# Performance work log

Measured on AMD Instinct MI355X. Metric: run time of the kernel, lower is better.

The kernel has to match this reference:

```python
import jax, jax.numpy as jnp
import numpy as np

B, ENC_LEN, DEC_LEN = 4, 1024, 256
ENC_H, DEC_H, ATTN = 1024, 1024, 256


def setup_inputs() -> dict:
    key = jax.random.key(0)
    k1, k2, k3, k4, k5, k6 = jax.random.split(key, 6)
    scale = 0.02
    return {
        "encoded_seq": jax.random.normal(k1, (B, ENC_LEN, ENC_H), jnp.float32),
        "decoder_state": jax.random.normal(k2, (B, DEC_LEN, DEC_H), jnp.float32),
        "input_pad_mask": jnp.ones((B, ENC_LEN), jnp.float32),
        "Wh": jax.random.normal(k3, (ENC_H, ATTN), jnp.float32) * scale,
        "Ws": jax.random.normal(k4, (DEC_H, ATTN), jnp.float32) * scale,
        "bs": jax.random.normal(k5, (ATTN,), jnp.float32) * scale,
        "v": jax.random.normal(k6, (ATTN,), jnp.float32) * scale,
    }


def reference(encoded_seq, decoder_state, input_pad_mask, Wh, Ws, bs, v):
    # projections: [B, dec, A] and [B, enc, A]
    proj_dec = jnp.einsum('bdh,ha->bda', decoder_state, Ws) + bs
    proj_enc = jnp.einsum('beh,ha->bea', encoded_seq, Wh)
    # additive score: tanh(broadcast add) then dot with selector vector v
    added = jnp.tanh(proj_dec[:, :, None, :] + proj_enc[:, None, :, :])  # [B,dec,enc,A]
    attn_logits = jnp.einsum('bdea,a->bde', added, v)                    # [B,dec,enc]
    attn_weights = jax.nn.softmax(attn_logits, axis=-1)
    attn_weights2 = attn_weights * input_pad_mask[:, None, :]
    attn_renorm = attn_weights2 / jnp.sum(attn_weights2, axis=-1, keepdims=True)
    context = jnp.einsum('bde,beh->bdh', attn_renorm, encoded_seq)       # [B,dec,enc_h]
    return context, attn_renorm
```

## Files before the change

### kernel.cpp

```cpp
#include <hip/hip_runtime.h>
#include <hip/hip_bf16.h>

#define BB 4
#define ENC_LEN 1024
#define DEC_LEN 256
#define ENC_H 1024
#define ATTN_A 256

#define C2F 2.8853900817779268f

typedef short bf16x8 __attribute__((ext_vector_type(8)));
typedef float f32x4 __attribute__((ext_vector_type(4)));
typedef unsigned int u32x2 __attribute__((ext_vector_type(2)));

union Q2D {
  uint4 q;
  u32x2 d[2];
};
union BF8 {
  u32x2 d[2];
  bf16x8 v;
};

static __device__ __forceinline__ unsigned short f2bf(float x) {
  union {
    float f;
    unsigned int u;
  } c;
  c.f = x;
  unsigned int r = c.u + 0x7FFFu + ((c.u >> 16) & 1u);
  return (unsigned short)(r >> 16);
}

__global__ __launch_bounds__(256) void prep_k(
    const float* __restrict__ Wh, const float* __restrict__ Ws,
    const float* __restrict__ enc, const float* __restrict__ dec,
    unsigned short* __restrict__ WhT, unsigned short* __restrict__ WsT,
    unsigned short* __restrict__ encT, unsigned short* __restrict__ encB,
    unsigned short* __restrict__ decB) {
  __shared__ unsigned short T[64][68];
  const int wb = blockIdx.x;
  const int t = threadIdx.x;
  const int lr = t >> 4;
  const int lc4 = (t & 15) * 4;

  if (wb >= 1152) {
    const int q = wb - 1152;
    const int r0 = (q >> 4) * 64;
    const int c0 = (q & 15) * 64;
#pragma unroll
    for (int p = 0; p < 4; ++p) {
      const int r = lr + p * 16;
      const float4 v = *(const float4*)&dec[(long)(r0 + r) * ENC_H + c0 + lc4];
      ushort4 o;
      o.x = f2bf(v.x);
      o.y = f2bf(v.y);
      o.z = f2bf(v.z);
      o.w = f2bf(v.w);
      *(ushort4*)&decB[(long)(r0 + r) * ENC_H + c0 + lc4] = o;
    }
    return;
  }

  const float* in;
  unsigned short* out;
  unsigned short* out2 = nullptr;
  int R, C, bx, by;
  if (wb < 128) {
    in = (wb < 64) ? Wh : Ws;
    out = (wb < 64) ? WhT : WsT;
    const int tt = wb & 63;
    R = ENC_H;
    C = ATTN_A;
    bx = tt & 3;
    by = tt >> 2;
  } else {
    const int tt0 = wb - 128;
    const int b = tt0 >> 8;
    const int tt = tt0 & 255;
    in = enc + (long)b * ENC_LEN * ENC_H;
    out = encT + (long)b * ENC_H * ENC_LEN;
    out2 = encB + (long)b * ENC_LEN * ENC_H;
    R = ENC_LEN;
    C = ENC_H;
    bx = tt & 15;
    by = tt >> 4;
  }
  const int r0 = by * 64;
  const int c0 = bx * 64;

#pragma unroll
  for (int p = 0; p < 4; ++p) {
    const int r = lr + p * 16;
    const float4 v = *(const float4*)&in[(long)(r0 + r) * C + c0 + lc4];
    ushort4 o;
    o.x = f2bf(v.x);
    o.y = f2bf(v.y);
    o.z = f2bf(v.z);
    o.w = f2bf(v.w);
    *(ushort4*)&T[r][lc4] = o;
    if (out2) *(ushort4*)&out2[(long)(r0 + r) * C + c0 + lc4] = o;
  }
  __syncthreads();
#pragma unroll
  for (int p = 0; p < 4; ++p) {
    const int c = lr + p * 16;
    ushort4 o;
    o.x = T[lc4 + 0][c];
    o.y = T[lc4 + 1][c];
    o.z = T[lc4 + 2][c];
    o.w = T[lc4 + 3][c];
    *(ushort4*)&out[(long)(c0 + c) * R + r0 + lc4] = o;
  }
}

__global__ __launch_bounds__(256) void pgemm(const unsigned short* __restrict__ decB,
                                             const unsigned short* __restrict__ encB,
                                             const unsigned short* __restrict__ WsT,
                                             const unsigned short* __restrict__ WhT,
                                             float* __restrict__ pdP,
                                             float* __restrict__ peP) {
  __shared__ unsigned short As[64][36];
  __shared__ unsigned short Bs[64][36];
  __shared__ float Cs[64][68];

  const int s = blockIdx.z;
  const bool isPD = blockIdx.y < 16;
  const unsigned short* A = isPD ? decB : encB;
  const unsigned short* BT = isPD ? WsT : WhT;
  const int m0 = (isPD ? blockIdx.y : (blockIdx.y - 16)) * 64;
  const int n0 = blockIdx.x * 64;
  const int kb = s * 512;

  const int tid = threadIdx.x;
  const int lane = tid & 63;
  const int wave = tid >> 6;
  const int quad = lane >> 4;
  const int l16 = lane & 15;
  const int wm = (wave >> 1) * 32;
  const int wn = (wave & 1) * 32;
  const int sr = tid >> 2;
  const int sk = (tid & 3) * 8;

  f32x4 acc[2][2] = {{{0.f, 0.f, 0.f, 0.f}, {0.f, 0.f, 0.f, 0.f}},
                     {{0.f, 0.f, 0.f, 0.f}, {0.f, 0.f, 0.f, 0.f}}};

  const unsigned short* Ap = A + (long)(m0 + sr) * ENC_H + kb + sk;
  const unsigned short* Bp = BT + (long)(n0 + sr) * ENC_H + kb + sk;

  Q2D av, bv;
  av.q = *(const uint4*)(Ap);
  bv.q = *(const uint4*)(Bp);

  for (int k0 = 0; k0 < 512; k0 += 32) {
    __syncthreads();
    *(u32x2*)&As[sr][sk] = av.d[0];
    *(u32x2*)&As[sr][sk + 4] = av.d[1];
    *(u32x2*)&Bs[sr][sk] = bv.d[0];
    *(u32x2*)&Bs[sr][sk + 4] = bv.d[1];
    const int kn = (k0 + 32 < 512) ? (k0 + 32) : 0;
    av.q = *(const uint4*)(Ap + kn);
    bv.q = *(const uint4*)(Bp + kn);
    __syncthreads();

    bf16x8 af[2], bfr[2];
#pragma unroll
    for (int i = 0; i < 2; ++i) {
      BF8 t;
      t.d[0] = *(const u32x2*)&As[wm + i * 16 + l16][quad * 8];
      t.d[1] = *(const u32x2*)&As[wm + i * 16 + l16][quad * 8 + 4];
      af[i] = t.v;
    }
#pragma unroll
    for (int j = 0; j < 2; ++j) {
      BF8 t;
      t.d[0] = *(const u32x2*)&Bs[wn + j * 16 + l16][quad * 8];
      t.d[1] = *(const u32x2*)&Bs[wn + j * 16 + l16][quad * 8 + 4];
      bfr[j] = t.v;
    }
#pragma unroll
    for (int i = 0; i < 2; ++i)
#pragma unroll
      for (int j = 0; j < 2; ++j)
        acc[i][j] = __builtin_amdgcn_mfma_f32_16x16x32_bf16(af[i], bfr[j], acc[i][j],
                                                            0, 0, 0);
  }

  if (isPD) {
    float* out = pdP + (long)s * (1024 * ATTN_A);
#pragma unroll
    for (int j = 0; j < 2; ++j) {
      const int col = n0 + wn + j * 16 + l16;
#pragma unroll
      for (int i = 0; i < 2; ++i) {
        const int row = m0 + wm + i * 16 + quad * 4;
#pragma unroll
        for (int r = 0; r < 4; ++r)
          out[(long)(row + r) * ATTN_A + col] = C2F * acc[i][j][r];
      }
    }
  } else {
    __syncthreads();
#pragma unroll
    for (int i = 0; i < 2; ++i)
#pragma unroll
      for (int j = 0; j < 2; ++j)
#pragma unroll
        for (int r = 0; r < 4; ++r)
          Cs[wn + j * 16 + l16][wm + i * 16 + quad * 4 + r] = C2F * acc[i][j][r];
    __syncthreads();
    const int gb = m0 >> 10;
    const int e0 = m0 & 1023;
    float* out = peP + (long)s * (BB * ATTN_A * ENC_LEN);
#pragma unroll
    for (int p = 0; p < 4; ++p) {
      const int arow = (tid >> 4) + p * 16;
      const int e4 = (tid & 15) * 4;
      const float4 o = *(const float4*)&Cs[arow][e4];
      *(float4*)&out[(long)gb * (ATTN_A * ENC_LEN) + (long)(n0 + arow) * ENC_LEN +
                     e0 + e4] = o;
    }
  }
}

__global__ __launch_bounds__(256) void logits_k(const float* __restrict__ peP,
                                                const float* __restrict__ pdP,
                                                const float* __restrict__ v,
                                                const float* __restrict__ bs,
                                                float* __restrict__ p0,
                                                float* __restrict__ p1) {
  const int tid = threadIdx.x;
  const int e = blockIdx.x * 256 + tid;
  const int d0 = blockIdx.y * 8;
  const int b = blockIdx.z >> 1;
  const int a0 = (blockIdx.z & 1) * 128;

  __shared__ float Ed[128][8];
  __shared__ float vv[128];

  if (tid < 128) {
    const float cb = C2F * bs[a0 + tid];
#pragma unroll
    for (int dd = 0; dd < 8; ++dd) {
      const long idx = (long)(b * DEC_LEN + d0 + dd) * ATTN_A + a0 + tid;
      const float t = pdP[idx] + pdP[idx + 1024 * ATTN_A] + cb;
      Ed[tid][dd] = __builtin_amdgcn_exp2f(t);
    }
    vv[tid] = -2.0f * v[a0 + tid];
  }
  __syncthreads();

  float acc[8] = {0.f, 0.f, 0.f, 0.f, 0.f, 0.f, 0.f, 0.f};
  const float* pe0 = peP + (long)b * (ATTN_A * ENC_LEN) + (long)a0 * ENC_LEN + e;
  const float* pe1 = pe0 + (long)BB * ATTN_A * ENC_LEN;

  float pn0[4], pn1[4];
#pragma unroll
  for (int u = 0; u < 4; ++u) {
    pn0[u] = pe0[(long)u * ENC_LEN];
    pn1[u] = pe1[(long)u * ENC_LEN];
  }

  for (int a4 = 0; a4 < 128; a4 += 4) {
    float Ee[4];
#pragma unroll
    for (int u = 0; u < 4; ++u) Ee[u] = __builtin_amdgcn_exp2f(pn0[u] + pn1[u]);
    const int an = (a4 + 4 < 128) ? (a4 + 4) : 0;
#pragma unroll
    for (int u = 0; u < 4; ++u) {
      pn0[u] = pe0[(long)(an + u) * ENC_LEN];
      pn1[u] = pe1[(long)(an + u) * ENC_LEN];
    }
    const float4 v4 = *(const float4*)&vv[a4];

    float ed[4][8];
#pragma unroll
    for (int u = 0; u < 4; ++u) {
      const float4 e0v = *(const float4*)&Ed[a4 + u][0];
      const float4 e1v = *(const float4*)&Ed[a4 + u][4];
      ed[u][0] = e0v.x;
      ed[u][1] = e0v.y;
      ed[u][2] = e0v.z;
      ed[u][3] = e0v.w;
      ed[u][4] = e1v.x;
      ed[u][5] = e1v.y;
      ed[u][6] = e1v.z;
      ed[u][7] = e1v.w;
    }

#pragma unroll
    for (int dd = 0; dd < 8; ++dd) {
      const float dn0 = fmaf(ed[0][dd], Ee[0], 1.0f);
      const float dn1 = fmaf(ed[1][dd], Ee[1], 1.0f);
      const float dn2 = fmaf(ed[2][dd], Ee[2], 1.0f);
      const float dn3 = fmaf(ed[3][dd], Ee[3], 1.0f);
      const float x12 = dn0 * dn1;
      const float x34 = dn2 * dn3;
      float t1 = v4.x * dn1;
      t1 = fmaf(v4.y, dn0, t1);
      float t2 = v4.z * dn3;
      t2 = fmaf(v4.w, dn2, t2);
      float num = t1 * x34;
      num = fmaf(t2, x12, num);
      const float D = x12 * x34;
      const float r = __builtin_amdgcn_rcpf(D);
      acc[dd] = fmaf(num, r, acc[dd]);
    }
  }

  float* po = (blockIdx.z & 1) ? p1 : p0;
  const long base = ((long)(b * DEC_LEN + d0) * ENC_LEN) + e;
#pragma unroll
  for (int dd = 0; dd < 8; ++dd) po[base + (long)dd * ENC_LEN] = acc[dd];
}

__global__ __launch_bounds__(256) void softmax2_k(float* __restrict__ p0,
                                                  const float* __restrict__ p1,
                                                  const float* __restrict__ mask,
                                                  unsigned short* __restrict__ attnB) {
  const int row = blockIdx.x;
  const int b = row >> 8;
  const int tid = threadIdx.x;
  float* rp = p0 + (long)row * ENC_LEN;
  const float* rq = p1 + (long)row * ENC_LEN;
  const float* mp = mask + b * ENC_LEN;
  unsigned short* rb = attnB + (long)row * ENC_LEN;

  float l[4], m[4];
#pragma unroll
  for (int j = 0; j < 4; ++j) {
    l[j] = rp[tid + 256 * j] + rq[tid + 256 * j];
    m[j] = mp[tid + 256 * j];
  }

  __shared__ float redmax[4];
  __shared__ float redsum[4];
  const int lane = tid & 63;
  const int wid = tid >> 6;

  float tm = fmaxf(fmaxf(l[0], l[1]), fmaxf(l[2], l[3]));
#pragma unroll
  for (int off = 1; off < 64; off <<= 1) tm = fmaxf(tm, __shfl_xor(tm, off, 64));
  if (lane == 0) redmax[wid] = tm;
  __syncthreads();
  const float rmax = fmaxf(fmaxf(redmax[0], redmax[1]), fmaxf(redmax[2], redmax[3]));

  const float LOG2E = 1.4426950408889634f;
  float p[4];
  float ts = 0.f;
#pragma unroll
  for (int j = 0; j < 4; ++j) {
    p[j] = __builtin_amdgcn_exp2f((l[j] - rmax) * LOG2E) * m[j];
    ts += p[j];
  }
#pragma unroll
  for (int off = 1; off < 64; off <<= 1) ts += __shfl_xor(ts, off, 64);
  if (lane == 0) redsum[wid] = ts;
  __syncthreads();
  const float rsum = redsum[0] + redsum[1] + redsum[2] + redsum[3];

  const float inv = 1.0f / rsum;
#pragma unroll
  for (int j = 0; j < 4; ++j) {
    const float w = p[j] * inv;
    rp[tid + 256 * j] = w;
    rb[tid + 256 * j] = f2bf(w);
  }
}

__global__ __launch_bounds__(256) void cgemm(const unsigned short* __restrict__ attnB,
                                             const unsigned short* __restrict__ encT,
                                             float* __restrict__ cP) {
  __shared__ unsigned short As[64][36];
  __shared__ unsigned short Bs[64][36];

  const int b = blockIdx.z >> 1;
  const int s = blockIdx.z & 1;
  const int kb = s * 512;
  const unsigned short* A = attnB + (long)b * DEC_LEN * ENC_LEN;
  const unsigned short* BT = encT + (long)b * ENC_H * ENC_LEN;
  float* C = cP + (long)s * (BB * DEC_LEN * ENC_H) + (long)b * DEC_LEN * ENC_H;

  const int tid = threadIdx.x;
  const int lane = tid & 63;
  const int wave = tid >> 6;
  const int quad = lane >> 4;
  const int l16 = lane & 15;
  const int wm = (wave >> 1) * 32;
  const int wn = (wave & 1) * 32;
  const int m0 = blockIdx.y * 64;
  const int n0 = blockIdx.x * 64;
  const int sr = tid >> 2;
  const int sk = (tid & 3) * 8;

  f32x4 acc[2][2] = {{{0.f, 0.f, 0.f, 0.f}, {0.f, 0.f, 0.f, 0.f}},
                     {{0.f, 0.f, 0.f, 0.f}, {0.f, 0.f, 0.f, 0.f}}};

  const unsigned short* Ap = A + (long)(m0 + sr) * ENC_LEN + kb + sk;
  const unsigned short* Bp = BT + (long)(n0 + sr) * ENC_LEN + kb + sk;

  Q2D av, bv;
  av.q = *(const uint4*)(Ap);
  bv.q = *(const uint4*)(Bp);

  for (int k0 = 0; k0 < 512; k0 += 32) {
    __syncthreads();
    *(u32x2*)&As[sr][sk] = av.d[0];
    *(u32x2*)&As[sr][sk + 4] = av.d[1];
    *(u32x2*)&Bs[sr][sk] = bv.d[0];
    *(u32x2*)&Bs[sr][sk + 4] = bv.d[1];
    const int kn = (k0 + 32 < 512) ? (k0 + 32) : 0;
    av.q = *(const uint4*)(Ap + kn);
    bv.q = *(const uint4*)(Bp + kn);
    __syncthreads();

    bf16x8 af[2], bfr[2];
#pragma unroll
    for (int i = 0; i < 2; ++i) {
      BF8 t;
      t.d[0] = *(const u32x2*)&As[wm + i * 16 + l16][quad * 8];
      t.d[1] = *(const u32x2*)&As[wm + i * 16 + l16][quad * 8 + 4];
      af[i] = t.v;
    }
#pragma unroll
    for (int j = 0; j < 2; ++j) {
      BF8 t;
      t.d[0] = *(const u32x2*)&Bs[wn + j * 16 + l16][quad * 8];
      t.d[1] = *(const u32x2*)&Bs[wn + j * 16 + l16][quad * 8 + 4];
      bfr[j] = t.v;
    }
#pragma unroll
    for (int i = 0; i < 2; ++i)
#pragma unroll
      for (int j = 0; j < 2; ++j)
        acc[i][j] = __builtin_amdgcn_mfma_f32_16x16x32_bf16(af[i], bfr[j], acc[i][j],
                                                            0, 0, 0);
  }

#pragma unroll
  for (int j = 0; j < 2; ++j) {
    const int col = n0 + wn + j * 16 + l16;
#pragma unroll
    for (int i = 0; i < 2; ++i) {
      const int row = m0 + wm + i * 16 + quad * 4;
#pragma unroll
      for (int r = 0; r < 4; ++r) C[(long)(row + r) * ENC_H + col] = acc[i][j][r];
    }
  }
}

__global__ __launch_bounds__(256) void creduce(const float* __restrict__ cP,
                                               float* __restrict__ ctx) {
  const long i = ((long)blockIdx.x * 256 + threadIdx.x) * 4;
  const float4 x = *(const float4*)&cP[i];
  const float4 y = *(const float4*)&cP[i + (long)BB * DEC_LEN * ENC_H];
  float4 o;
  o.x = x.x + y.x;
  o.y = x.y + y.y;
  o.z = x.z + y.z;
  o.w = x.w + y.w;
  *(float4*)&ctx[i] = o;
}

template <int OMODE, bool BIAS>
__global__ __launch_bounds__(256) void gemm64(const float* __restrict__ A,
                                              const float* __restrict__ B,
                                              const float* __restrict__ bias,
                                              float* __restrict__ C,
                                              int K, int lda, int ldb, int ldc,
                                              long sA, long sB, long sC) {
  const int bz = blockIdx.z;
  A += (long)bz * sA;
  B += (long)bz * sB;
  C += (long)bz * sC;

  const int tid = threadIdx.x;
  const int tx = tid & 15;
  const int ty = tid >> 4;

  __shared__ float As2[16][64];
  __shared__ float Bs2[16][64];

  float acc[4][4];
#pragma unroll
  for (int i = 0; i < 4; ++i)
#pragma unroll
    for (int j = 0; j < 4; ++j) acc[i][j] = 0.f;

  const int ar = tid >> 2;
  const int ak4 = (tid & 3) << 2;
  const int br = tid >> 4;
  const int bn4 = (tid & 15) << 2;

  const float* Aload = A + (long)(blockIdx.y * 64 + ar) * lda + ak4;
  const float* Bload = B + (long)br * ldb + blockIdx.x * 64 + bn4;

  for (int k0 = 0; k0 < K; k0 += 16) {
    const float4 av = *(const float4*)(Aload + k0);
    const float4 bv = *(const float4*)(Bload + (long)k0 * ldb);
    __syncthreads();
    As2[ak4 + 0][ar] = av.x;
    As2[ak4 + 1][ar] = av.y;
    As2[ak4 + 2][ar] = av.z;
    As2[ak4 + 3][ar] = av.w;
    *(float4*)&Bs2[br][bn4] = bv;
    __syncthreads();
#pragma unroll
    for (int kk = 0; kk < 16; ++kk) {
      const float4 a4 = *(const float4*)&As2[kk][ty << 2];
      const float4 b4 = *(const float4*)&Bs2[kk][tx << 2];
      const float am[4] = {a4.x, a4.y, a4.z, a4.w};
      const float bn[4] = {b4.x, b4.y, b4.z, b4.w};
#pragma unroll
      for (int i = 0; i < 4; ++i)
#pragma unroll
        for (int j = 0; j < 4; ++j) acc[i][j] = fmaf(am[i], bn[j], acc[i][j]);
    }
  }

  if (OMODE == 0) {
    const int row0 = blockIdx.y * 64 + (ty << 2);
    const int col0 = blockIdx.x * 64 + (tx << 2);
    float4 bb4 = make_float4(0.f, 0.f, 0.f, 0.f);
    if (BIAS) bb4 = *(const float4*)&bias[col0];
#pragma unroll
    for (int i = 0; i < 4; ++i) {
      float4 o;
      o.x = acc[i][0] + bb4.x;
      o.y = acc[i][1] + bb4.y;
      o.z = acc[i][2] + bb4.z;
      o.w = acc[i][3] + bb4.w;
      *(float4*)&C[(long)(row0 + i) * ldc + col0] = o;
    }
  } else {
#pragma unroll
    for (int i = 0; i < 4; ++i) {
      const int gr = blockIdx.y * 64 + (ty << 2) + i;
      const int b = gr >> 10;
      const int e = gr & 1023;
#pragma unroll
      for (int j = 0; j < 4; ++j) {
        const int col = blockIdx.x * 64 + (tx << 2) + j;
        C[(long)b * (ATTN_A * ENC_LEN) + (long)col * ENC_LEN + e] = acc[i][j];
      }
    }
  }
}

__global__ __launch_bounds__(256) void logits_fb(const float* __restrict__ peT,
                                                 const float* __restrict__ pd,
                                                 const float* __restrict__ v,
                                                 float* __restrict__ out) {
  const int tid = threadIdx.x;
  const int e = blockIdx.x * 256 + tid;
  const int d0 = blockIdx.y * 8;
  const int b = blockIdx.z;

  __shared__ float cpd[ATTN_A][8];
  __shared__ float vv[ATTN_A];

  {
    const int a = tid;
#pragma unroll
    for (int dd = 0; dd < 8; ++dd)
      cpd[a][dd] = C2F * pd[((b * DEC_LEN + d0 + dd) * ATTN_A) + a];
    vv[a] = -2.0f * v[a];
  }
  __syncthreads();

  float acc[8] = {0.f, 0.f, 0.f, 0.f, 0.f, 0.f, 0.f, 0.f};
  const float* pe = peT + (long)b * (ATTN_A * ENC_LEN) + e;

  for (int a = 0; a < ATTN_A; a += 4) {
    float pes[4];
#pragma unroll
    for (int u = 0; u < 4; ++u) pes[u] = pe[(long)(a + u) * ENC_LEN];
#pragma unroll
    for (int u = 0; u < 4; ++u) {
      const float cpe = C2F * pes[u];
      const float vu = vv[a + u];
      const float4 c0 = *(const float4*)&cpd[a + u][0];
      const float4 c1 = *(const float4*)&cpd[a + u][4];
      const float cd[8] = {c0.x, c0.y, c0.z, c0.w, c1.x, c1.y, c1.z, c1.w};
#pragma unroll
      for (int dd = 0; dd < 8; ++dd) {
        const float x = cd[dd] + cpe;
        const float ex = __builtin_amdgcn_exp2f(x);
        const float r = __builtin_amdgcn_rcpf(ex + 1.0f);
        acc[dd] = fmaf(vu, r, acc[dd]);
      }
    }
  }

  const long base = ((long)(b * DEC_LEN + d0) * ENC_LEN) + e;
#pragma unroll
  for (int dd = 0; dd < 8; ++dd) out[base + (long)dd * ENC_LEN] = acc[dd];
}

__global__ __launch_bounds__(256) void softmax_fb(float* __restrict__ attn,
                                                  const float* __restrict__ mask) {
  const int row = blockIdx.x;
  const int b = row >> 8;
  const int tid = threadIdx.x;
  float* rp = attn + (long)row * ENC_LEN;
  const float* mp = mask + b * ENC_LEN;

  float l[4], m[4];
#pragma unroll
  for (int j = 0; j < 4; ++j) {
    l[j] = rp[tid + 256 * j];
    m[j] = mp[tid + 256 * j];
  }

  __shared__ float redmax[4];
  __shared__ float redsum[4];
  const int lane = tid & 63;
  const int wid = tid >> 6;

  float tm = fmaxf(fmaxf(l[0], l[1]), fmaxf(l[2], l[3]));
#pragma unroll
  for (int off = 1; off < 64; off <<= 1) tm = fmaxf(tm, __shfl_xor(tm, off, 64));
  if (lane == 0) redmax[wid] = tm;
  __syncthreads();
  const float rmax = fmaxf(fmaxf(redmax[0], redmax[1]), fmaxf(redmax[2], redmax[3]));

  const float LOG2E = 1.4426950408889634f;
  float p[4];
  float ts = 0.f;
#pragma unroll
  for (int j = 0; j < 4; ++j) {
    p[j] = __builtin_amdgcn_exp2f((l[j] - rmax) * LOG2E) * m[j];
    ts += p[j];
  }
#pragma unroll
  for (int off = 1; off < 64; off <<= 1) ts += __shfl_xor(ts, off, 64);
  if (lane == 0) redsum[wid] = ts;
  __syncthreads();
  const float rsum = redsum[0] + redsum[1] + redsum[2] + redsum[3];

  const float inv = 1.0f / rsum;
#pragma unroll
  for (int j = 0; j < 4; ++j) rp[tid + 256 * j] = p[j] * inv;
}

extern "C" void kernel_launch(void* const* d_in, const int* in_sizes, int n_in,
                              void* d_out, int out_size, void* d_ws, size_t ws_size,
                              hipStream_t stream) {
  const float* enc = (const float*)d_in[0];
  const float* dec = (const float*)d_in[1];
  const float* mask = (const float*)d_in[2];
  const float* Wh = (const float*)d_in[3];
  const float* Ws = (const float*)d_in[4];
  const float* bs = (const float*)d_in[5];
  const float* v = (const float*)d_in[6];

  float* ctx = (float*)d_out;
  float* attn = ctx + (long)BB * DEC_LEN * ENC_H;

  const long N_PD = 2L * 1024 * ATTN_A;
  const long N_PE = 2L * BB * ATTN_A * ENC_LEN;
  const long N_P1 = (long)BB * DEC_LEN * ENC_LEN;
  const long N_CP = 2L * BB * DEC_LEN * ENC_H;
  const long N_ENC = (long)BB * ENC_H * ENC_LEN;
  const long N_W = (long)ATTN_A * ENC_H;
  const long N_DEC = 1024L * ENC_H;
  const long N_ATT = (long)BB * DEC_LEN * ENC_LEN;
  const size_t FAST_WS = (N_PD + N_PE + N_P1 + N_CP) * 4 +
                         (N_ENC + 2 * N_W + N_ENC + N_DEC + N_ATT) * 2;

  if (ws_size >= FAST_WS) {
    float* pdP = (float*)d_ws;
    float* peP = pdP + N_PD;
    float* p1 = peP + N_PE;
    float* cP = p1 + N_P1;
    unsigned short* encT = (unsigned short*)(cP + N_CP);
    unsigned short* WhT = encT + N_ENC;
    unsigned short* WsT = WhT + N_W;
    unsigned short* encB = WsT + N_W;
    unsigned short* decB = encB + N_ENC;
    unsigned short* attnB = decB + N_DEC;

    prep_k<<<dim3(1408, 1, 1), 256, 0, stream>>>(Wh, Ws, enc, dec, WhT, WsT, encT,
                                                 encB, decB);
    pgemm<<<dim3(4, 80, 2), 256, 0, stream>>>(decB, encB, WsT, WhT, pdP, peP);
    logits_k<<<dim3(4, 32, BB * 2), 256, 0, stream>>>(peP, pdP, v, bs, attn, p1);
    softmax2_k<<<dim3(BB * DEC_LEN, 1, 1), 256, 0, stream>>>(attn, p1, mask, attnB);
    cgemm<<<dim3(16, 4, BB * 2), 256, 0, stream>>>(attnB, encT, cP);
    creduce<<<dim3(1024, 1, 1), 256, 0, stream>>>(cP, ctx);
  } else {
    float* pd = (float*)d_ws;
    float* peT = pd + (long)BB * DEC_LEN * ATTN_A;

    gemm64<0, true><<<dim3(ATTN_A / 64, (BB * DEC_LEN) / 64, 1), 256, 0, stream>>>(
        dec, Ws, bs, pd, ENC_H, ENC_H, ATTN_A, ATTN_A, 0, 0, 0);
    gemm64<1, false><<<dim3(ATTN_A / 64, (BB * ENC_LEN) / 64, 1), 256, 0, stream>>>(
        enc, Wh, nullptr, peT, ENC_H, ENC_H, ATTN_A, 0, 0, 0, 0);
    logits_fb<<<dim3(ENC_LEN / 256, DEC_LEN / 8, BB), 256, 0, stream>>>(peT, pd, v,
                                                                        attn);
    softmax_fb<<<dim3(BB * DEC_LEN, 1, 1), 256, 0, stream>>>(attn, mask);
    gemm64<0, false><<<dim3(ENC_H / 64, DEC_LEN / 64, BB), 256, 0, stream>>>(
        attn, enc, nullptr, ctx, ENC_LEN, ENC_LEN, ENC_H, ENC_H,
        (long)DEC_LEN * ENC_LEN, (long)ENC_LEN * ENC_H, (long)DEC_LEN * ENC_H);
  }
}
```

Measured before the change: 143.3 us.

## Process 16 decoder rows per logits block with transposed shared exp table

The logits kernel now handles 16 decoder positions per block instead of 8, halving the grid's y dimension, so each encoder-projection exp computed per thread is reused across twice as many decoder rows. The decoder exp table is transposed to [16][128] so each inner-loop step reads a float4 across four attention indices for one decoder row, and all 256 threads fill it instead of 128. This cuts global reads and exp work on the encoder projection per output, at the cost of more accumulator registers and fewer blocks (512 instead of 1024), which may lower occupancy.

```diff
diff --git a/kernel.cpp b/kernel.cpp
--- a/kernel.cpp
+++ b/kernel.cpp
@@ -231,26 +231,32 @@
                                                 float* __restrict__ p1) {
   const int tid = threadIdx.x;
   const int e = blockIdx.x * 256 + tid;
-  const int d0 = blockIdx.y * 8;
+  const int d0 = blockIdx.y * 16;
   const int b = blockIdx.z >> 1;
   const int a0 = (blockIdx.z & 1) * 128;
 
-  __shared__ float Ed[128][8];
+  __shared__ float EdT[16][128];
   __shared__ float vv[128];
 
-  if (tid < 128) {
-    const float cb = C2F * bs[a0 + tid];
-#pragma unroll
-    for (int dd = 0; dd < 8; ++dd) {
-      const long idx = (long)(b * DEC_LEN + d0 + dd) * ATTN_A + a0 + tid;
-      const float t = pdP[idx] + pdP[idx + 1024 * ATTN_A] + cb;
-      Ed[tid][dd] = __builtin_amdgcn_exp2f(t);
-    }
-    vv[tid] = -2.0f * v[a0 + tid];
+  {
+    const int a = tid & 127;
+    const int dh = tid >> 7;
+    const float cb = C2F * bs[a0 + a];
+#pragma unroll
+    for (int j = 0; j < 8; ++j) {
+      const int dd = dh * 8 + j;
+      const long idx = (long)(b * DEC_LEN + d0 + dd) * ATTN_A + a0 + a;
+      EdT[dd][a] =
+          __builtin_amdgcn_exp2f(pdP[idx] + pdP[idx + 1024 * ATTN_A] + cb);
+    }
+    if (dh == 0) vv[a] = -2.0f * v[a0 + a];
   }
   __syncthreads();
 
-  float acc[8] = {0.f, 0.f, 0.f, 0.f, 0.f, 0.f, 0.f, 0.f};
+  float acc[16];
+#pragma unroll
+  for (int i = 0; i < 16; ++i) acc[i] = 0.f;
+
   const float* pe0 = peP + (long)b * (ATTN_A * ENC_LEN) + (long)a0 * ENC_LEN + e;
   const float* pe1 = pe0 + (long)BB * ATTN_A * ENC_LEN;
 
@@ -273,27 +279,13 @@
     }
     const float4 v4 = *(const float4*)&vv[a4];
 
-    float ed[4][8];
-#pragma unroll
-    for (int u = 0; u < 4; ++u) {
-      const float4 e0v = *(const float4*)&Ed[a4 + u][0];
-      const float4 e1v = *(const float4*)&Ed[a4 + u][4];
-      ed[u][0] = e0v.x;
-      ed[u][1] = e0v.y;
-      ed[u][2] = e0v.z;
-      ed[u][3] = e0v.w;
-      ed[u][4] = e1v.x;
-      ed[u][5] = e1v.y;
-      ed[u][6] = e1v.z;
-      ed[u][7] = e1v.w;
-    }
-
-#pragma unroll
-    for (int dd = 0; dd < 8; ++dd) {
-      const float dn0 = fmaf(ed[0][dd], Ee[0], 1.0f);
-      const float dn1 = fmaf(ed[1][dd], Ee[1], 1.0f);
-      const float dn2 = fmaf(ed[2][dd], Ee[2], 1.0f);
-      const float dn3 = fmaf(ed[3][dd], Ee[3], 1.0f);
+#pragma unroll
+    for (int dd = 0; dd < 16; ++dd) {
+      const float4 ed = *(const float4*)&EdT[dd][a4];
+      const float dn0 = fmaf(ed.x, Ee[0], 1.0f);
+      const float dn1 = fmaf(ed.y, Ee[1], 1.0f);
+      const float dn2 = fmaf(ed.z, Ee[2], 1.0f);
+      const float dn3 = fmaf(ed.w, Ee[3], 1.0f);
       const float x12 = dn0 * dn1;
       const float x34 = dn2 * dn3;
       float t1 = v4.x * dn1;
@@ -311,7 +303,7 @@
   float* po = (blockIdx.z & 1) ? p1 : p0;
   const long base = ((long)(b * DEC_LEN + d0) * ENC_LEN) + e;
 #pragma unroll
-  for (int dd = 0; dd < 8; ++dd) po[base + (long)dd * ENC_LEN] = acc[dd];
+  for (int dd = 0; dd < 16; ++dd) po[base + (long)dd * ENC_LEN] = acc[dd];
 }
 
 __global__ __launch_bounds__(256) void softmax2_k(float* __restrict__ p0,
@@ -683,7 +675,7 @@
     prep_k<<<dim3(1408, 1, 1), 256, 0, stream>>>(Wh, Ws, enc, dec, WhT, WsT, encT,
                                                  encB, decB);
     pgemm<<<dim3(4, 80, 2), 256, 0, stream>>>(decB, encB, WsT, WhT, pdP, peP);
-    logits_k<<<dim3(4, 32, BB * 2), 256, 0, stream>>>(peP, pdP, v, bs, attn, p1);
+    logits_k<<<dim3(4, 16, BB * 2), 256, 0, stream>>>(peP, pdP, v, bs, attn, p1);
     softmax2_k<<<dim3(BB * DEC_LEN, 1, 1), 256, 0, stream>>>(attn, p1, mask, attnB);
     cgemm<<<dim3(16, 4, BB * 2), 256, 0, stream>>>(attnB, encT, cP);
     creduce<<<dim3(1024, 1, 1), 256, 0, stream>>>(cP, ctx);
```

Result: slower. 146.4 us (+2.2%).
